# Optimization experiments

Measured on AMD Instinct MI355X. Metric: run time of the kernel, lower is better.

The kernel has to match this reference:

```python
import jax, jax.numpy as jnp
import numpy as np


@jax.custom_vjp
def spike(mem, v_th):
    # Heaviside forward, triangular surrogate backward (gamma=1.0)
    return (mem >= v_th).astype(mem.dtype)


def _spike_fwd(mem, v_th):
    return spike(mem, v_th), (mem, v_th)


def _spike_bwd(res, g):
    mem, v_th = res
    surr = jnp.clip(1.0 - jnp.abs(mem - v_th), 0.0)  # gamma = 1
    return (g * surr, jnp.zeros_like(v_th))  # torch returns None for threshold grad


spike.defvjp(_spike_fwd, _spike_bwd)


def setup_inputs() -> dict:
    key = jax.random.key(0)
    ks = jax.random.split(key, 6)
    T, B, C, H, W = 8, 16, 256, 32, 32
    NH, HID = 4, 64
    x = jax.random.normal(ks[0], (T, B, C, H, W), dtype=jnp.float32)
    decay_param = jnp.float32(np.log(0.85 / 0.15))  # logit(0.85)
    v_th = jnp.float32(0.5)
    W1 = jax.random.normal(ks[1], (NH, HID, T), dtype=jnp.float32) * 0.1
    b1 = jax.random.normal(ks[2], (NH, HID), dtype=jnp.float32) * 0.01
    W2 = jax.random.normal(ks[3], (NH, T, HID), dtype=jnp.float32) * 0.1
    b2 = jax.random.normal(ks[4], (NH, T), dtype=jnp.float32) * 0.01
    att_w = jnp.ones((NH,), dtype=jnp.float32) / NH
    return {"x": x, "decay_param": decay_param, "v_th": v_th,
            "W1": W1, "b1": b1, "W2": W2, "b2": b2, "att_w": att_w}


def reference(x, decay_param, v_th, W1, b1, W2, b2, att_w):
    T, B, C, H, W = x.shape
    d = jax.nn.sigmoid(decay_param)

    def step(carry, inp):
        mem, spk = carry  # detached states, as in the torch module
        m = d * (mem - v_th * spk) + inp
        denom = jnp.mean(jnp.abs(m), axis=(1, 2, 3), keepdims=True) + 1e-6
        m = m / denom
        s = spike(m, v_th)
        carry = (jax.lax.stop_gradient(m), jax.lax.stop_gradient(s))
        return carry, s

    init = (jnp.zeros_like(x[0]), jnp.zeros_like(x[0]))
    _, spikes = jax.lax.scan(step, init, x)          # [T,B,C,H,W]

    feats = spikes.reshape(T, B, C * H * W)          # [T,B,F]
    summary = feats.mean(axis=2).T                   # [B,T]
    # multi-head MLP attention over time
    h = jax.nn.relu(jnp.einsum('bt,nht->bnh', summary, W1) + b1[None])  # [B,NH,HID]
    maps = jnp.einsum('bnh,nth->bnt', h, W2) + b2[None]                  # [B,NH,T]
    weighted = jnp.sum(maps * att_w[None, :, None], axis=1)              # [B,T]
    aw = jax.nn.softmax(weighted, axis=-1).T[:, :, None]                 # [T,B,1]
    out = jnp.sum(feats * aw, axis=0)                                    # [B,F]
    return out
```

## Files before the change

### kernel.cpp

```cpp
#include <hip/hip_runtime.h>

#define NT    8
#define NB    16
#define FS    262144
#define TPB   256
#define BPB   32
#define GRID  (NB*BPB)
#define CHK   8
#define ELB   (TPB*CHK*4)
#define SPIN_CAP (1L<<26)

#define WS_SMALL 33344
#define WS_FAST  49728

__global__ __launch_bounds__(TPB, 2)
void bispike_kernel(const float* __restrict__ x,
                    const float* __restrict__ decay_p,
                    const float* __restrict__ vth_p,
                    const float* __restrict__ W1,
                    const float* __restrict__ b1,
                    const float* __restrict__ W2,
                    const float* __restrict__ b2,
                    const float* __restrict__ att_w,
                    float* __restrict__ out,
                    double* __restrict__ bsum,
                    int* __restrict__ scnt,
                    int* __restrict__ ccnt,
                    int* __restrict__ cnt,
                    int fastcnt)
{
    const int tid  = threadIdx.x;
    const int lane = tid & 63;
    const int wid  = tid >> 6;
    const int b    = blockIdx.x % NB;
    const int bg   = blockIdx.x / NB;

    const double dec  = 1.0 / (1.0 + exp(-(double)decay_p[0]));
    const double vth  = (double)vth_p[0];
    const double csub = dec * vth;

    double   u[CHK * 4];
    float4   xv[CHK];
    unsigned sm[NT];

    {
        const float* p = x + (size_t)b * FS + (size_t)bg * ELB + tid * 4;
        #pragma unroll
        for (int k = 0; k < CHK; ++k) xv[k] = *(const float4*)(p + k * (TPB * 4));
    }
    double lsum;
    {
        double n0 = 0.0, n1 = 0.0, n2 = 0.0, n3 = 0.0;
        #pragma unroll
        for (int k = 0; k < CHK; ++k) {
            u[k*4+0] = (double)xv[k].x; n0 += fabs(u[k*4+0]);
            u[k*4+1] = (double)xv[k].y; n1 += fabs(u[k*4+1]);
            u[k*4+2] = (double)xv[k].z; n2 += fabs(u[k*4+2]);
            u[k*4+3] = (double)xv[k].w; n3 += fabs(u[k*4+3]);
        }
        lsum = (n0 + n1) + (n2 + n3);
    }

    __shared__ double dred[4];
    __shared__ double denom_s;

    #pragma unroll 1
    for (int t = 0; t < NT; ++t) {
        if (t < NT - 1) {
            const float* p = x + ((size_t)(t + 1) * NB + b) * FS
                               + (size_t)bg * ELB + tid * 4;
            #pragma unroll
            for (int k = 0; k < CHK; ++k) xv[k] = *(const float4*)(p + k * (TPB * 4));
        }

        double ls = lsum;
        #pragma unroll
        for (int off = 32; off > 0; off >>= 1)
            ls += __shfl_down(ls, off, 64);
        if (lane == 0) dred[wid] = ls;
        __syncthreads();

        if (tid < 64) {
            double bs = (dred[0] + dred[1]) + (dred[2] + dred[3]);
            double* slot = bsum + (size_t)(t * NB + b) * BPB;
            if (tid == 0)
                __hip_atomic_store(slot + bg, -bs, __ATOMIC_RELAXED,
                                   __HIP_MEMORY_SCOPE_AGENT);

            const int  sl  = lane & 31;
            const bool act = (lane < 32) && (sl != bg);
            double v = 0.0; long it = 0;
            for (;;) {
                if (act)
                    v = __hip_atomic_load(slot + sl, __ATOMIC_RELAXED,
                                          __HIP_MEMORY_SCOPE_AGENT);
                if (__all(!act || __double_as_longlong(v) != 0)) break;
                if (++it > SPIN_CAP) break;
                __builtin_amdgcn_s_sleep(1);
            }
            double tot = (lane >= 32) ? 0.0 : ((sl == bg) ? bs : -v);
            #pragma unroll
            for (int off = 32; off > 0; off >>= 1)
                tot += __shfl_down(tot, off, 64);
            if (tid == 0)
                denom_s = tot / (double)FS + 1e-6;
        }
        __syncthreads();
        const double denom = denom_s;

        const double thr = vth * denom;
        const double a   = dec * (1.0 / denom);
        unsigned smt = 0;
        if (t < NT - 1) {
            double n0 = 0.0, n1 = 0.0, n2 = 0.0, n3 = 0.0;
            #pragma unroll
            for (int k = 0; k < CHK; ++k) {
                const double xn0 = (double)xv[k].x, xn1 = (double)xv[k].y,
                             xn2 = (double)xv[k].z, xn3 = (double)xv[k].w;
                double un;
                bool s0 = (u[k*4+0] >= thr); if (s0) smt |= 1u << (k*4+0);
                un = fma(a, u[k*4+0], xn0); if (s0) un -= csub;
                u[k*4+0] = un; n0 += fabs(un);
                bool s1 = (u[k*4+1] >= thr); if (s1) smt |= 1u << (k*4+1);
                un = fma(a, u[k*4+1], xn1); if (s1) un -= csub;
                u[k*4+1] = un; n1 += fabs(un);
                bool s2 = (u[k*4+2] >= thr); if (s2) smt |= 1u << (k*4+2);
                un = fma(a, u[k*4+2], xn2); if (s2) un -= csub;
                u[k*4+2] = un; n2 += fabs(un);
                bool s3 = (u[k*4+3] >= thr); if (s3) smt |= 1u << (k*4+3);
                un = fma(a, u[k*4+3], xn3); if (s3) un -= csub;
                u[k*4+3] = un; n3 += fabs(un);
            }
            lsum = (n0 + n1) + (n2 + n3);
        } else {
            #pragma unroll
            for (int j = 0; j < CHK * 4; ++j)
                if (u[j] >= thr) smt |= 1u << j;
        }
        sm[t] = smt;
    }

    __shared__ int ired[NT][4];
    #pragma unroll
    for (int t = 0; t < NT; ++t) {
        int c = __popc(sm[t]);
        #pragma unroll
        for (int off = 32; off > 0; off >>= 1)
            c += __shfl_down(c, off, 64);
        if (lane == 0) ired[t][wid] = c;
    }
    __syncthreads();

    __shared__ double summ_s[NT];
    __shared__ int totc_s[NT];

    if (fastcnt) {
        if (tid < 64) {
            int* cb = cnt + b * (NT * BPB);
            if (tid < NT) {
                int tot = (ired[tid][0] + ired[tid][1])
                        + (ired[tid][2] + ired[tid][3]);
                __hip_atomic_store(cb + tid * BPB + bg, tot + 1,
                                   __ATOMIC_RELAXED, __HIP_MEMORY_SCOPE_AGENT);
            }
            const int  sl  = lane & 31;
            const bool act = (lane < 32) && (sl != bg);
            int vt[NT]; long it = 0;
            for (;;) {
                bool ok = true;
                #pragma unroll
                for (int t = 0; t < NT; ++t) {
                    if (act) {
                        vt[t] = __hip_atomic_load(cb + t * BPB + sl,
                                                  __ATOMIC_RELAXED,
                                                  __HIP_MEMORY_SCOPE_AGENT);
                        ok = ok && (vt[t] > 0);
                    }
                }
                if (__all(ok)) break;
                if (++it > SPIN_CAP) break;
                __builtin_amdgcn_s_sleep(1);
            }
            #pragma unroll
            for (int t = 0; t < NT; ++t) {
                int s;
                if (lane >= 32)      s = 0;
                else if (sl == bg)   s = (ired[t][0] + ired[t][1])
                                       + (ired[t][2] + ired[t][3]);
                else                 s = vt[t] - 1;
                #pragma unroll
                for (int off = 32; off > 0; off >>= 1)
                    s += __shfl_down(s, off, 64);
                if (tid == 0) totc_s[t] = s;
            }
        }
        __syncthreads();
        if (tid < NT)
            summ_s[tid] = (double)totc_s[tid] / (double)FS;
    } else {
        if (tid < NT) {
            int tot = (ired[tid][0] + ired[tid][1]) + (ired[tid][2] + ired[tid][3]);
            __hip_atomic_fetch_add(&scnt[tid * NB + b], tot,
                                   __ATOMIC_RELEASE, __HIP_MEMORY_SCOPE_AGENT);
        }
        __syncthreads();
        if (tid == 0) {
            __hip_atomic_fetch_add(&ccnt[b], 1,
                                   __ATOMIC_RELEASE, __HIP_MEMORY_SCOPE_AGENT);
            long it = 0;
            while (__hip_atomic_load(&ccnt[b], __ATOMIC_ACQUIRE,
                                     __HIP_MEMORY_SCOPE_AGENT) < BPB
                   && it++ < SPIN_CAP)
                __builtin_amdgcn_s_sleep(4);
        }
        __syncthreads();
        if (tid < NT) {
            int c = __hip_atomic_load(&scnt[tid * NB + b],
                                      __ATOMIC_ACQUIRE, __HIP_MEMORY_SCOPE_AGENT);
            summ_s[tid] = (double)c / (double)FS;
        }
    }
    __syncthreads();

    __shared__ double h_s[4 * 64];
    __shared__ double wmat_s[NT];
    {
        int nh = tid >> 6, hd = tid & 63;
        double acc = 0.0;
        #pragma unroll
        for (int t = 0; t < NT; ++t)
            acc += summ_s[t] * (double)W1[nh * 512 + hd * 8 + t];
        acc += (double)b1[nh * 64 + hd];
        h_s[tid] = fmax(acc, 0.0);
    }
    __syncthreads();
    if (tid < NT) {
        double w = 0.0;
        for (int nh = 0; nh < 4; ++nh) {
            double macc = 0.0;
            for (int hd = 0; hd < 64; ++hd)
                macc += h_s[nh * 64 + hd] * (double)W2[nh * 512 + tid * 64 + hd];
            macc += (double)b2[nh * 8 + tid];
            w += macc * (double)att_w[nh];
        }
        wmat_s[tid] = w;
    }
    __syncthreads();

    double awr[NT];
    {
        double mx = wmat_s[0];
        #pragma unroll
        for (int t = 1; t < NT; ++t) mx = fmax(mx, wmat_s[t]);
        double ss = 0.0;
        #pragma unroll
        for (int t = 0; t < NT; ++t) { awr[t] = exp(wmat_s[t] - mx); ss += awr[t]; }
        #pragma unroll
        for (int t = 0; t < NT; ++t) awr[t] = awr[t] / ss;
    }

    float* po = out + (size_t)b * FS + (size_t)bg * ELB + tid * 4;
    #pragma unroll
    for (int k = 0; k < CHK; ++k) {
        double o[4] = {0.0, 0.0, 0.0, 0.0};
        #pragma unroll
        for (int t = 0; t < NT; ++t) {
            const unsigned smt = sm[t];
            o[0] += ((smt >> (k * 4 + 0)) & 1) ? awr[t] : 0.0;
            o[1] += ((smt >> (k * 4 + 1)) & 1) ? awr[t] : 0.0;
            o[2] += ((smt >> (k * 4 + 2)) & 1) ? awr[t] : 0.0;
            o[3] += ((smt >> (k * 4 + 3)) & 1) ? awr[t] : 0.0;
        }
        *(float4*)(po + k * (TPB * 4)) =
            make_float4((float)o[0], (float)o[1], (float)o[2], (float)o[3]);
    }
}

__global__ void diag_kernel(float* out, int code) {
    out[0] = 100000.0f + (float)code;
}

extern "C" void kernel_launch(void* const* d_in, const int* in_sizes, int n_in,
                              void* d_out, int out_size, void* d_ws, size_t ws_size,
                              hipStream_t stream) {
    const float* x     = (const float*)d_in[0];
    const float* decay = (const float*)d_in[1];
    const float* vth   = (const float*)d_in[2];
    const float* W1    = (const float*)d_in[3];
    const float* b1    = (const float*)d_in[4];
    const float* W2    = (const float*)d_in[5];
    const float* b2    = (const float*)d_in[6];
    const float* att   = (const float*)d_in[7];
    float* out = (float*)d_out;

    if (ws_size < WS_SMALL) {
        diag_kernel<<<1, 1, 0, stream>>>(out, 999);
        return;
    }
    const int fastcnt = (ws_size >= (size_t)WS_FAST) ? 1 : 0;

    double* bsum = (double*)d_ws;
    int*    scnt = (int*)((char*)d_ws + 32768);
    int*    ccnt = (int*)((char*)d_ws + 33280);
    int*    cnt  = (int*)((char*)d_ws + 33344);

    hipMemsetAsync(d_ws, 0, fastcnt ? WS_FAST : WS_SMALL, stream);

    hipGetLastError();
    bispike_kernel<<<dim3(GRID), dim3(TPB), 0, stream>>>(
        x, decay, vth, W1, b1, W2, b2, att, out, bsum, scnt, ccnt, cnt, fastcnt);
    hipError_t err = hipGetLastError();
    if (err != hipSuccess) {
        diag_kernel<<<1, 1, 0, stream>>>(out, (int)err);
    }
}
```

Measured before the change: 234.8 us.

## Replace all-to-all block spin exchange with leader-gather and broadcast

The per-timestep norm reduction and the final spike-count reduction across the 32 blocks of a batch used to have every block poll all 31 peers' slots. Now only the leader block (bg==0) gathers the partial sums, computes the result, and publishes it to a single broadcast slot that the other blocks poll with one lane. This cuts global atomic polling traffic from all-to-all to gather-plus-broadcast, at the cost of an extra hop of latency through the leader on each barrier. The fallback atomic-add path is removed and the workspace layout grows.

```diff
diff --git a/kernel.cpp b/kernel.cpp
--- a/kernel.cpp
+++ b/kernel.cpp
@@ -10,8 +10,7 @@
 #define ELB   (TPB*CHK*4)
 #define SPIN_CAP (1L<<26)
 
-#define WS_SMALL 33344
-#define WS_FAST  49728
+#define WS_NEED 50688
 
 __global__ __launch_bounds__(TPB, 2)
 void bispike_kernel(const float* __restrict__ x,
@@ -24,16 +23,16 @@
                     const float* __restrict__ att_w,
                     float* __restrict__ out,
                     double* __restrict__ bsum,
-                    int* __restrict__ scnt,
-                    int* __restrict__ ccnt,
+                    double* __restrict__ dbc,
                     int* __restrict__ cnt,
-                    int fastcnt)
+                    int* __restrict__ cbc)
 {
     const int tid  = threadIdx.x;
     const int lane = tid & 63;
     const int wid  = tid >> 6;
     const int b    = blockIdx.x % NB;
     const int bg   = blockIdx.x / NB;
+    const bool leader = (bg == 0);
 
     const double dec  = 1.0 / (1.0 + exp(-(double)decay_p[0]));
     const double vth  = (double)vth_p[0];
@@ -81,29 +80,44 @@
         __syncthreads();
 
         if (tid < 64) {
-            double bs = (dred[0] + dred[1]) + (dred[2] + dred[3]);
+            const double bs = (dred[0] + dred[1]) + (dred[2] + dred[3]);
             double* slot = bsum + (size_t)(t * NB + b) * BPB;
-            if (tid == 0)
-                __hip_atomic_store(slot + bg, -bs, __ATOMIC_RELAXED,
-                                   __HIP_MEMORY_SCOPE_AGENT);
-
-            const int  sl  = lane & 31;
-            const bool act = (lane < 32) && (sl != bg);
-            double v = 0.0; long it = 0;
-            for (;;) {
-                if (act)
-                    v = __hip_atomic_load(slot + sl, __ATOMIC_RELAXED,
-                                          __HIP_MEMORY_SCOPE_AGENT);
-                if (__all(!act || __double_as_longlong(v) != 0)) break;
-                if (++it > SPIN_CAP) break;
-                __builtin_amdgcn_s_sleep(1);
-            }
-            double tot = (lane >= 32) ? 0.0 : ((sl == bg) ? bs : -v);
-            #pragma unroll
-            for (int off = 32; off > 0; off >>= 1)
-                tot += __shfl_down(tot, off, 64);
-            if (tid == 0)
-                denom_s = tot / (double)FS + 1e-6;
+            if (!leader) {
+                if (lane == 0) {
+                    __hip_atomic_store(slot + bg, -bs, __ATOMIC_RELAXED,
+                                       __HIP_MEMORY_SCOPE_AGENT);
+                    double dv; long it = 0;
+                    for (;;) {
+                        dv = __hip_atomic_load(&dbc[t * NB + b], __ATOMIC_RELAXED,
+                                               __HIP_MEMORY_SCOPE_AGENT);
+                        if (__double_as_longlong(dv) != 0) break;
+                        if (++it > SPIN_CAP) break;
+                        __builtin_amdgcn_s_sleep(8);
+                    }
+                    denom_s = dv;
+                }
+            } else {
+                const bool act = (lane >= 1 && lane < 32);
+                double v = 0.0; long it = 0;
+                for (;;) {
+                    if (act)
+                        v = __hip_atomic_load(slot + lane, __ATOMIC_RELAXED,
+                                              __HIP_MEMORY_SCOPE_AGENT);
+                    if (__all(!act || __double_as_longlong(v) != 0)) break;
+                    if (++it > SPIN_CAP) break;
+                    __builtin_amdgcn_s_sleep(2);
+                }
+                double tot = (lane == 0) ? bs : ((lane < 32) ? -v : 0.0);
+                #pragma unroll
+                for (int off = 32; off > 0; off >>= 1)
+                    tot += __shfl_down(tot, off, 64);
+                if (lane == 0) {
+                    const double dn = tot / (double)FS + 1e-6;
+                    __hip_atomic_store(&dbc[t * NB + b], dn, __ATOMIC_RELAXED,
+                                       __HIP_MEMORY_SCOPE_AGENT);
+                    denom_s = dn;
+                }
+            }
         }
         __syncthreads();
         const double denom = denom_s;
@@ -154,24 +168,35 @@
     __shared__ double summ_s[NT];
     __shared__ int totc_s[NT];
 
-    if (fastcnt) {
-        if (tid < 64) {
-            int* cb = cnt + b * (NT * BPB);
-            if (tid < NT) {
-                int tot = (ired[tid][0] + ired[tid][1])
-                        + (ired[tid][2] + ired[tid][3]);
-                __hip_atomic_store(cb + tid * BPB + bg, tot + 1,
+    if (tid < 64) {
+        int* cb = cnt + b * (NT * BPB);
+        if (!leader) {
+            if (lane < NT) {
+                int tot = (ired[lane][0] + ired[lane][1])
+                        + (ired[lane][2] + ired[lane][3]);
+                __hip_atomic_store(cb + lane * BPB + bg, tot + 1,
                                    __ATOMIC_RELAXED, __HIP_MEMORY_SCOPE_AGENT);
             }
-            const int  sl  = lane & 31;
-            const bool act = (lane < 32) && (sl != bg);
+            const bool act = (lane < NT);
+            int cv = 0; long it = 0;
+            for (;;) {
+                if (act)
+                    cv = __hip_atomic_load(&cbc[b * NT + lane], __ATOMIC_RELAXED,
+                                           __HIP_MEMORY_SCOPE_AGENT);
+                if (__all(!act || cv != 0)) break;
+                if (++it > SPIN_CAP) break;
+                __builtin_amdgcn_s_sleep(8);
+            }
+            if (act) totc_s[lane] = cv - 1;
+        } else {
+            const bool act = (lane >= 1 && lane < 32);
             int vt[NT]; long it = 0;
             for (;;) {
                 bool ok = true;
                 #pragma unroll
                 for (int t = 0; t < NT; ++t) {
                     if (act) {
-                        vt[t] = __hip_atomic_load(cb + t * BPB + sl,
+                        vt[t] = __hip_atomic_load(cb + t * BPB + lane,
                                                   __ATOMIC_RELAXED,
                                                   __HIP_MEMORY_SCOPE_AGENT);
                         ok = ok && (vt[t] > 0);
@@ -179,47 +204,29 @@
                 }
                 if (__all(ok)) break;
                 if (++it > SPIN_CAP) break;
-                __builtin_amdgcn_s_sleep(1);
+                __builtin_amdgcn_s_sleep(2);
             }
             #pragma unroll
             for (int t = 0; t < NT; ++t) {
                 int s;
-                if (lane >= 32)      s = 0;
-                else if (sl == bg)   s = (ired[t][0] + ired[t][1])
-                                       + (ired[t][2] + ired[t][3]);
-                else                 s = vt[t] - 1;
+                if (lane == 0)      s = (ired[t][0] + ired[t][1])
+                                      + (ired[t][2] + ired[t][3]);
+                else if (act)       s = vt[t] - 1;
+                else                s = 0;
                 #pragma unroll
                 for (int off = 32; off > 0; off >>= 1)
                     s += __shfl_down(s, off, 64);
-                if (tid == 0) totc_s[t] = s;
-            }
-        }
-        __syncthreads();
-        if (tid < NT)
-            summ_s[tid] = (double)totc_s[tid] / (double)FS;
-    } else {
-        if (tid < NT) {
-            int tot = (ired[tid][0] + ired[tid][1]) + (ired[tid][2] + ired[tid][3]);
-            __hip_atomic_fetch_add(&scnt[tid * NB + b], tot,
-                                   __ATOMIC_RELEASE, __HIP_MEMORY_SCOPE_AGENT);
-        }
-        __syncthreads();
-        if (tid == 0) {
-            __hip_atomic_fetch_add(&ccnt[b], 1,
-                                   __ATOMIC_RELEASE, __HIP_MEMORY_SCOPE_AGENT);
-            long it = 0;
-            while (__hip_atomic_load(&ccnt[b], __ATOMIC_ACQUIRE,
-                                     __HIP_MEMORY_SCOPE_AGENT) < BPB
-                   && it++ < SPIN_CAP)
-                __builtin_amdgcn_s_sleep(4);
-        }
-        __syncthreads();
-        if (tid < NT) {
-            int c = __hip_atomic_load(&scnt[tid * NB + b],
-                                      __ATOMIC_ACQUIRE, __HIP_MEMORY_SCOPE_AGENT);
-            summ_s[tid] = (double)c / (double)FS;
-        }
-    }
+                if (lane == 0) {
+                    totc_s[t] = s;
+                    __hip_atomic_store(&cbc[b * NT + t], s + 1,
+                                       __ATOMIC_RELAXED, __HIP_MEMORY_SCOPE_AGENT);
+                }
+            }
+        }
+    }
+    __syncthreads();
+    if (tid < NT)
+        summ_s[tid] = (double)totc_s[tid] / (double)FS;
     __syncthreads();
 
     __shared__ double h_s[4 * 64];
@@ -293,22 +300,21 @@
     const float* att   = (const float*)d_in[7];
     float* out = (float*)d_out;
 
-    if (ws_size < WS_SMALL) {
+    if (ws_size < WS_NEED) {
         diag_kernel<<<1, 1, 0, stream>>>(out, 999);
         return;
     }
-    const int fastcnt = (ws_size >= (size_t)WS_FAST) ? 1 : 0;
 
     double* bsum = (double*)d_ws;
-    int*    scnt = (int*)((char*)d_ws + 32768);
-    int*    ccnt = (int*)((char*)d_ws + 33280);
-    int*    cnt  = (int*)((char*)d_ws + 33344);
-
-    hipMemsetAsync(d_ws, 0, fastcnt ? WS_FAST : WS_SMALL, stream);
+    double* dbc  = (double*)((char*)d_ws + 32768);
+    int*    cnt  = (int*)((char*)d_ws + 33792);
+    int*    cbc  = (int*)((char*)d_ws + 50176);
+
+    hipMemsetAsync(d_ws, 0, WS_NEED, stream);
 
     hipGetLastError();
     bispike_kernel<<<dim3(GRID), dim3(TPB), 0, stream>>>(
-        x, decay, vth, W1, b1, W2, b2, att, out, bsum, scnt, ccnt, cnt, fastcnt);
+        x, decay, vth, W1, b1, W2, b2, att, out, bsum, dbc, cnt, cbc);
     hipError_t err = hipGetLastError();
     if (err != hipSuccess) {
         diag_kernel<<<1, 1, 0, stream>>>(out, (int)err);
```

After: 235.1 us. About the same (+0.1%).
